# Kernel optimization log

Hardware: AMD Instinct MI355X
Metric: run time of the kernel (lower is better)

Reference implementation:

```python
import jax, jax.numpy as jnp
import numpy as np

B, T, C, H = 8, 2048, 1024, 64

def setup_inputs() -> dict:
    key = jax.random.key(0)
    k1, k2, k3, k4 = jax.random.split(key, 4)
    x = jax.random.normal(k1, (B, T, C), dtype=jnp.float32)
    # torch nn.Linear default init ~ U(-1/sqrt(in), 1/sqrt(in)); scale kept small for stability
    s = 1.0 / np.sqrt(C)
    Wq = jax.random.uniform(k2, (C, H), dtype=jnp.float32, minval=-s, maxval=s)
    Wk = jax.random.uniform(k3, (C, H), dtype=jnp.float32, minval=-s, maxval=s)
    Wv = jax.random.uniform(k4, (C, H), dtype=jnp.float32, minval=-s, maxval=s)
    return {"x": x, "Wq": Wq, "Wk": Wk, "Wv": Wv}

def reference(x, Wq, Wk, Wv):
    # x: [B,T,C]; Wq/Wk/Wv: [C,H] (equivalent to torch Linear weight transposed)
    Q = jnp.einsum('btc,ch->bth', x, Wq)
    K = jnp.einsum('btc,ch->bth', x, Wk)
    V = jnp.einsum('btc,ch->bth', x, Wv)
    H_ = Q.shape[-1]
    scale = 1.0 / jnp.sqrt(jnp.asarray(H_, dtype=Q.dtype))
    w = jnp.einsum('bqh,bkh->bqk', Q, K) * scale  # [B,T,T]
    T_ = x.shape[1]
    causal = jnp.tril(jnp.ones((T_, T_), dtype=bool))
    w = jnp.where(causal, w, -jnp.inf)
    w = jax.nn.softmax(w, axis=-1)
    out = jnp.einsum('bqk,bkh->bqh', w, V)  # [B,T,H]
    return out
```

## Files before the change

kernel.cpp:

```cpp
#include <hip/hip_runtime.h>
#include <math.h>

#define Bb 8
#define Tt 2048
#define Cc 1024
#define Hh 64
#define BT (Bb * Tt)
#define SLOG2E 0.18033688011112042f

typedef __attribute__((ext_vector_type(8))) short short8;
typedef __attribute__((ext_vector_type(4))) float floatx4;

__device__ inline unsigned short f2bf(float f) {
  unsigned int u = __builtin_bit_cast(unsigned int, f);
  u += 0x7fff + ((u >> 16) & 1);
  return (unsigned short)(u >> 16);
}
__device__ inline float bf2f(unsigned short u) {
  unsigned int x = ((unsigned int)u) << 16;
  return __builtin_bit_cast(float, x);
}

__global__ __launch_bounds__(256) void wconv(
    const float* __restrict__ Wq, const float* __restrict__ Wk,
    const float* __restrict__ Wv, unsigned short* __restrict__ WT) {
  __shared__ __align__(16) float Ttile[32][68];
  int bid = blockIdx.x;
  int w = bid >> 5;
  int c0 = (bid & 31) * 32;
  const float* __restrict__ W = (w == 0) ? Wq : (w == 1 ? Wk : Wv);
  int t = threadIdx.x;
  {
    int i = t >> 3, h0 = (t & 7) * 8;
    float4 a = *(const float4*)&W[(size_t)(c0 + i) * Hh + h0];
    float4 b = *(const float4*)&W[(size_t)(c0 + i) * Hh + h0 + 4];
    *(float4*)&Ttile[i][h0] = a;
    *(float4*)&Ttile[i][h0 + 4] = b;
  }
  __syncthreads();
  int h = t >> 2, jj = t & 3;
  unsigned short tmp[8];
#pragma unroll
  for (int ii = 0; ii < 8; ++ii) tmp[ii] = f2bf(Ttile[jj * 8 + ii][h]);
  unsigned short* dst = &WT[(size_t)(w * 64 + h) * Cc + c0 + jj * 8];
  *(ushort4*)dst = make_ushort4(tmp[0], tmp[1], tmp[2], tmp[3]);
  *(ushort4*)(dst + 4) = make_ushort4(tmp[4], tmp[5], tmp[6], tmp[7]);
}

__global__ __launch_bounds__(256) void qkv3(
    const float* __restrict__ x, const unsigned short* __restrict__ WT,
    unsigned short* __restrict__ Qb, unsigned short* __restrict__ Kb,
    unsigned short* __restrict__ VTb) {
  __shared__ __align__(16) unsigned short As[2 * 512];
  __shared__ __align__(16) unsigned short Bs[12 * 512];

  int mt = blockIdx.x;
  int t = threadIdx.x;
  int wv = t >> 6, lane = t & 63;
  int lrow = lane & 15, quad = lane >> 4;

  floatx4 acc[2][3];
#pragma unroll
  for (int m = 0; m < 2; ++m)
#pragma unroll
    for (int j = 0; j < 3; ++j)
#pragma unroll
      for (int r = 0; r < 4; ++r) acc[m][j][r] = 0.f;

  const float* xb = x + (size_t)mt * 32 * Cc;
  int arow = t >> 3, acg = t & 7;

  for (int kk = 0; kk < 32; ++kk) {
    int k0 = kk * 32;
    __syncthreads();
    {
      float4 v = *(const float4*)(xb + (size_t)arow * Cc + k0 + acg * 4);
      int di = (arow >> 4) * 512 + ((acg >> 1) * 16 + (arow & 15)) * 8 + (acg & 1) * 4;
      *(ushort4*)&As[di] = make_ushort4(f2bf(v.x), f2bf(v.y), f2bf(v.z), f2bf(v.w));
    }
#pragma unroll
    for (int i = 0; i < 3; ++i) {
      int task = t + i * 256;
      int kc = task & 3, n = task >> 2;
      int di = (n >> 4) * 512 + (kc * 16 + (n & 15)) * 8;
      *(uint4*)&Bs[di] = *(const uint4*)&WT[(size_t)n * Cc + k0 + kc * 8];
    }
    __syncthreads();
    short8 a0 = *(const short8*)&As[lane * 8];
    short8 a1 = *(const short8*)&As[512 + lane * 8];
#pragma unroll
    for (int j = 0; j < 3; ++j) {
      short8 b = *(const short8*)&Bs[(wv * 3 + j) * 512 + lane * 8];
      acc[0][j] = __builtin_amdgcn_mfma_f32_16x16x32_bf16(a0, b, acc[0][j], 0, 0, 0);
      acc[1][j] = __builtin_amdgcn_mfma_f32_16x16x32_bf16(a1, b, acc[1][j], 0, 0, 0);
    }
  }
#pragma unroll
  for (int m = 0; m < 2; ++m) {
#pragma unroll
    for (int j = 0; j < 3; ++j) {
      int nbase = (wv * 3 + j) * 16;
      int region = nbase >> 6;
      int row0 = mt * 32 + m * 16 + quad * 4;
      if (region == 2) {
        int h = nbase - 128 + lrow;
        *(ushort4*)&VTb[(size_t)h * BT + row0] =
            make_ushort4(f2bf(acc[m][j][0]), f2bf(acc[m][j][1]),
                         f2bf(acc[m][j][2]), f2bf(acc[m][j][3]));
      } else {
        unsigned short* dst = region ? Kb : Qb;
        int col = (nbase & 63) + lrow;
#pragma unroll
        for (int r = 0; r < 4; ++r)
          dst[(size_t)(row0 + r) * Hh + col] = f2bf(acc[m][j][r]);
      }
    }
  }
}

__global__ __launch_bounds__(512) void attn3(
    const unsigned short* __restrict__ Qb, const unsigned short* __restrict__ Kb,
    const unsigned short* __restrict__ VTb, float* __restrict__ out) {
  __shared__ __align__(16) unsigned char smem[33 * 1024];
  unsigned short* Pall = (unsigned short*)smem;
  unsigned short* Ocomb = (unsigned short*)smem;
  float* Lcomb = (float*)(smem + 32768);

  int bid = blockIdx.x;
  int b = bid >> 5;
  int j = bid & 31;
  int t = threadIdx.x;
  int wv = t >> 6, lane = t & 63;
  int lrow = lane & 15, quad = lane >> 4;

  unsigned short* Pw = Pall + wv * 2048;

  short8 ones;
#pragma unroll
  for (int i = 0; i < 8; ++i) ones[i] = (short)0x3F80;

  for (int half = 0; half < 2; ++half) {
    int qt = half ? (63 - j) : j;
    int q0 = qt * 32;
    int nkt = (qt >> 1) + 1;

    short8 aq[2][2];
#pragma unroll
    for (int qs = 0; qs < 2; ++qs)
#pragma unroll
      for (int kc = 0; kc < 2; ++kc)
        aq[qs][kc] = *(const short8*)
            &Qb[(size_t)(b * Tt + q0 + qs * 16 + lrow) * Hh + kc * 32 + quad * 8];

    floatx4 acc_o[2][4];
    floatx4 acc_l[2];
#pragma unroll
    for (int qs = 0; qs < 2; ++qs) {
#pragma unroll
      for (int r = 0; r < 4; ++r) acc_l[qs][r] = 0.f;
#pragma unroll
      for (int hs = 0; hs < 4; ++hs)
#pragma unroll
        for (int r = 0; r < 4; ++r) acc_o[qs][hs][r] = 0.f;
    }

    for (int kt = wv; kt < nkt; kt += 8) {
      int kbase = b * Tt + kt * 64;
      short8 kf[4][2], vf[4][2];
#pragma unroll
      for (int sn = 0; sn < 4; ++sn)
#pragma unroll
        for (int kc = 0; kc < 2; ++kc)
          kf[sn][kc] = *(const short8*)
              &Kb[(size_t)(kbase + sn * 16 + lrow) * Hh + kc * 32 + quad * 8];
#pragma unroll
      for (int hs = 0; hs < 4; ++hs)
#pragma unroll
        for (int kc = 0; kc < 2; ++kc)
          vf[hs][kc] = *(const short8*)
              &VTb[(size_t)(hs * 16 + lrow) * BT + kbase + kc * 32 + quad * 8];

      floatx4 s[2][4];
#pragma unroll
      for (int qs = 0; qs < 2; ++qs)
#pragma unroll
        for (int sn = 0; sn < 4; ++sn) {
          floatx4 z;
#pragma unroll
          for (int r = 0; r < 4; ++r) z[r] = 0.f;
          z = __builtin_amdgcn_mfma_f32_16x16x32_bf16(aq[qs][0], kf[sn][0], z, 0, 0, 0);
          z = __builtin_amdgcn_mfma_f32_16x16x32_bf16(aq[qs][1], kf[sn][1], z, 0, 0, 0);
          s[qs][sn] = z;
        }

      bool diag = (kt == nkt - 1);
#pragma unroll
      for (int qs = 0; qs < 2; ++qs)
#pragma unroll
        for (int sn = 0; sn < 4; ++sn) {
          int k5 = (sn & 1) * 16 + lrow;
          int slot = qs * 2 + (sn >> 1);
          int rlbase = (k5 >> 3) * 16;
#pragma unroll
          for (int r = 0; r < 4; ++r) {
            float v = s[qs][sn][r] * SLOG2E;
            if (diag) {
              int gk = kt * 64 + sn * 16 + lrow;
              int gq = q0 + qs * 16 + quad * 4 + r;
              if (gk > gq) v = -INFINITY;
            }
            float p = exp2f(v);
            Pw[slot * 512 + (rlbase + quad * 4 + r) * 8 + (k5 & 7)] = f2bf(p);
          }
        }

      short8 ap[2][2];
#pragma unroll
      for (int qs = 0; qs < 2; ++qs)
#pragma unroll
        for (int kc = 0; kc < 2; ++kc)
          ap[qs][kc] = *(const short8*)&Pw[(qs * 2 + kc) * 512 + lane * 8];

#pragma unroll
      for (int qs = 0; qs < 2; ++qs) {
        acc_l[qs] = __builtin_amdgcn_mfma_f32_16x16x32_bf16(ap[qs][0], ones, acc_l[qs], 0, 0, 0);
        acc_l[qs] = __builtin_amdgcn_mfma_f32_16x16x32_bf16(ap[qs][1], ones, acc_l[qs], 0, 0, 0);
#pragma unroll
        for (int hs = 0; hs < 4; ++hs) {
          acc_o[qs][hs] = __builtin_amdgcn_mfma_f32_16x16x32_bf16(ap[qs][0], vf[hs][0], acc_o[qs][hs], 0, 0, 0);
          acc_o[qs][hs] = __builtin_amdgcn_mfma_f32_16x16x32_bf16(ap[qs][1], vf[hs][1], acc_o[qs][hs], 0, 0, 0);
        }
      }
    }

#pragma unroll
    for (int qs = 0; qs < 2; ++qs)
#pragma unroll
      for (int hs = 0; hs < 4; ++hs) {
        int s8 = qs * 4 + hs;
        *(ushort4*)&Ocomb[((wv * 8 + s8) * 64 + lane) * 4] =
            make_ushort4(f2bf(acc_o[qs][hs][0]), f2bf(acc_o[qs][hs][1]),
                         f2bf(acc_o[qs][hs][2]), f2bf(acc_o[qs][hs][3]));
      }
    if (lrow == 0) {
#pragma unroll
      for (int qs = 0; qs < 2; ++qs)
#pragma unroll
        for (int r = 0; r < 4; ++r)
          Lcomb[wv * 32 + qs * 16 + quad * 4 + r] = acc_l[qs][r];
    }
    __syncthreads();

    {
      int qsub = wv >> 2, hs = wv & 3;
      float o[4] = {0.f, 0.f, 0.f, 0.f};
#pragma unroll
      for (int w = 0; w < 8; ++w) {
        ushort4 pk = *(const ushort4*)&Ocomb[((w * 8 + wv) * 64 + lane) * 4];
        o[0] += bf2f(pk.x); o[1] += bf2f(pk.y);
        o[2] += bf2f(pk.z); o[3] += bf2f(pk.w);
      }
#pragma unroll
      for (int r = 0; r < 4; ++r) {
        float lv = 0.f;
#pragma unroll
        for (int w = 0; w < 8; ++w)
          lv += Lcomb[w * 32 + qsub * 16 + quad * 4 + r];
        int row = q0 + qsub * 16 + quad * 4 + r;
        out[(size_t)(b * Tt + row) * Hh + hs * 16 + lrow] = o[r] / lv;
      }
    }
    __syncthreads();
  }
}

extern "C" void kernel_launch(void* const* d_in, const int* in_sizes, int n_in,
                              void* d_out, int out_size, void* d_ws, size_t ws_size,
                              hipStream_t stream) {
  const float* x = (const float*)d_in[0];
  const float* Wq = (const float*)d_in[1];
  const float* Wk = (const float*)d_in[2];
  const float* Wv = (const float*)d_in[3];
  float* out = (float*)d_out;

  unsigned short* WT = (unsigned short*)d_ws;
  unsigned short* Qb = WT + 192 * 1024;
  unsigned short* Kb = Qb + (size_t)BT * Hh;
  unsigned short* VTb = Kb + (size_t)BT * Hh;

  wconv<<<dim3(96), dim3(256), 0, stream>>>(Wq, Wk, Wv, WT);
  qkv3<<<dim3(512), dim3(256), 0, stream>>>(x, WT, Qb, Kb, VTb);
  attn3<<<dim3(256), dim3(512), 0, stream>>>(Qb, Kb, VTb, out);
}
```

Before: 149.6 us.

## Load QKV GEMM operands directly from global into registers, dropping LDS staging

The QKV projection kernel stops staging x and weight tiles through shared memory with two barriers per k-step. Instead each wave loads its MFMA fragments straight from global memory, converting x to bf16 in registers. The block grows to 512 threads in 8 waves split 2 (rows) by 4 (columns), each wave owning three 16x16 accumulators. This removes barrier and LDS traffic. In exchange, x rows are reloaded by four waves and the weight tiles by every block, with less coalesced per-lane 16/32-byte accesses.

```diff
diff --git a/kernel.cpp b/kernel.cpp
--- a/kernel.cpp
+++ b/kernel.cpp
@@ -47,73 +47,61 @@
   *(ushort4*)(dst + 4) = make_ushort4(tmp[4], tmp[5], tmp[6], tmp[7]);
 }
 
-__global__ __launch_bounds__(256) void qkv3(
+__global__ __launch_bounds__(512) void qkv4(
     const float* __restrict__ x, const unsigned short* __restrict__ WT,
     unsigned short* __restrict__ Qb, unsigned short* __restrict__ Kb,
     unsigned short* __restrict__ VTb) {
-  __shared__ __align__(16) unsigned short As[2 * 512];
-  __shared__ __align__(16) unsigned short Bs[12 * 512];
-
   int mt = blockIdx.x;
   int t = threadIdx.x;
   int wv = t >> 6, lane = t & 63;
   int lrow = lane & 15, quad = lane >> 4;
-
-  floatx4 acc[2][3];
-#pragma unroll
-  for (int m = 0; m < 2; ++m)
-#pragma unroll
-    for (int j = 0; j < 3; ++j)
-#pragma unroll
-      for (int r = 0; r < 4; ++r) acc[m][j][r] = 0.f;
-
-  const float* xb = x + (size_t)mt * 32 * Cc;
-  int arow = t >> 3, acg = t & 7;
-
+  int wm = wv & 1;
+  int wn = wv >> 1;
+
+  floatx4 acc[3];
+#pragma unroll
+  for (int j = 0; j < 3; ++j)
+#pragma unroll
+    for (int r = 0; r < 4; ++r) acc[j][r] = 0.f;
+
+  int row = mt * 32 + wm * 16 + lrow;
+  const float* xp = x + (size_t)row * Cc + quad * 8;
+  const unsigned short* wp[3];
+#pragma unroll
+  for (int j = 0; j < 3; ++j)
+    wp[j] = WT + (size_t)(wn * 48 + j * 16 + lrow) * Cc + quad * 8;
+
+#pragma unroll 2
   for (int kk = 0; kk < 32; ++kk) {
-    int k0 = kk * 32;
-    __syncthreads();
-    {
-      float4 v = *(const float4*)(xb + (size_t)arow * Cc + k0 + acg * 4);
-      int di = (arow >> 4) * 512 + ((acg >> 1) * 16 + (arow & 15)) * 8 + (acg & 1) * 4;
-      *(ushort4*)&As[di] = make_ushort4(f2bf(v.x), f2bf(v.y), f2bf(v.z), f2bf(v.w));
-    }
-#pragma unroll
-    for (int i = 0; i < 3; ++i) {
-      int task = t + i * 256;
-      int kc = task & 3, n = task >> 2;
-      int di = (n >> 4) * 512 + (kc * 16 + (n & 15)) * 8;
-      *(uint4*)&Bs[di] = *(const uint4*)&WT[(size_t)n * Cc + k0 + kc * 8];
-    }
-    __syncthreads();
-    short8 a0 = *(const short8*)&As[lane * 8];
-    short8 a1 = *(const short8*)&As[512 + lane * 8];
+    float4 v0 = *(const float4*)(xp + kk * 32);
+    float4 v1 = *(const float4*)(xp + kk * 32 + 4);
+    short8 a;
+    a[0] = (short)f2bf(v0.x); a[1] = (short)f2bf(v0.y);
+    a[2] = (short)f2bf(v0.z); a[3] = (short)f2bf(v0.w);
+    a[4] = (short)f2bf(v1.x); a[5] = (short)f2bf(v1.y);
+    a[6] = (short)f2bf(v1.z); a[7] = (short)f2bf(v1.w);
 #pragma unroll
     for (int j = 0; j < 3; ++j) {
-      short8 b = *(const short8*)&Bs[(wv * 3 + j) * 512 + lane * 8];
-      acc[0][j] = __builtin_amdgcn_mfma_f32_16x16x32_bf16(a0, b, acc[0][j], 0, 0, 0);
-      acc[1][j] = __builtin_amdgcn_mfma_f32_16x16x32_bf16(a1, b, acc[1][j], 0, 0, 0);
-    }
-  }
-#pragma unroll
-  for (int m = 0; m < 2; ++m) {
-#pragma unroll
-    for (int j = 0; j < 3; ++j) {
-      int nbase = (wv * 3 + j) * 16;
-      int region = nbase >> 6;
-      int row0 = mt * 32 + m * 16 + quad * 4;
-      if (region == 2) {
-        int h = nbase - 128 + lrow;
-        *(ushort4*)&VTb[(size_t)h * BT + row0] =
-            make_ushort4(f2bf(acc[m][j][0]), f2bf(acc[m][j][1]),
-                         f2bf(acc[m][j][2]), f2bf(acc[m][j][3]));
-      } else {
-        unsigned short* dst = region ? Kb : Qb;
-        int col = (nbase & 63) + lrow;
-#pragma unroll
-        for (int r = 0; r < 4; ++r)
-          dst[(size_t)(row0 + r) * Hh + col] = f2bf(acc[m][j][r]);
-      }
+      short8 b = *(const short8*)(wp[j] + kk * 32);
+      acc[j] = __builtin_amdgcn_mfma_f32_16x16x32_bf16(a, b, acc[j], 0, 0, 0);
+    }
+  }
+
+  int tok0 = mt * 32 + wm * 16 + quad * 4;
+#pragma unroll
+  for (int j = 0; j < 3; ++j) {
+    int nbase = wn * 48 + j * 16;
+    if (nbase >= 128) {
+      int h = nbase - 128 + lrow;
+      *(ushort4*)&VTb[(size_t)h * BT + tok0] =
+          make_ushort4(f2bf(acc[j][0]), f2bf(acc[j][1]),
+                       f2bf(acc[j][2]), f2bf(acc[j][3]));
+    } else {
+      unsigned short* dst = (nbase >= 64) ? Kb : Qb;
+      int col = (nbase & 63) + lrow;
+#pragma unroll
+      for (int r = 0; r < 4; ++r)
+        dst[(size_t)(tok0 + r) * Hh + col] = f2bf(acc[j][r]);
     }
   }
 }
@@ -289,6 +277,6 @@
   unsigned short* VTb = Kb + (size_t)BT * Hh;
 
   wconv<<<dim3(96), dim3(256), 0, stream>>>(Wq, Wk, Wv, WT);
-  qkv3<<<dim3(512), dim3(256), 0, stream>>>(x, WT, Qb, Kb, VTb);
+  qkv4<<<dim3(512), dim3(512), 0, stream>>>(x, WT, Qb, Kb, VTb);
   attn3<<<dim3(256), dim3(512), 0, stream>>>(Qb, Kb, VTb, out);
 }
```

Result: slower. 181.6 us (+21.4%).
